# Kernel optimization log

Hardware: AMD Instinct MI355X
Metric: run time of the kernel (lower is better)

The kernel has to match this reference:

```python
import jax, jax.numpy as jnp
import numpy as np

N = 100000
E = 1600000
F_IN = 128
HID = 128
C = 10
NEG_SLOPE = 0.2


def setup_inputs() -> dict:
    key = jax.random.key(0)
    ks = jax.random.split(key, 12)
    x = jax.random.normal(ks[0], (N, F_IN), dtype=jnp.float32)
    edge_index = jax.random.randint(ks[1], (2, E), 0, N, dtype=jnp.int64)
    batch = jnp.zeros((N,), dtype=jnp.int64)
    s1 = 1.0 / np.sqrt(F_IN)
    s2 = 1.0 / np.sqrt(HID)
    return {
        "x": x,
        "edge_index": edge_index,
        "batch": batch,
        "W1": jax.random.normal(ks[2], (F_IN, HID), dtype=jnp.float32) * s1,
        "a_src1": jax.random.normal(ks[3], (HID,), dtype=jnp.float32) * s2,
        "a_dst1": jax.random.normal(ks[4], (HID,), dtype=jnp.float32) * s2,
        "b1": jnp.zeros((HID,), dtype=jnp.float32),
        "W2": jax.random.normal(ks[5], (HID, HID), dtype=jnp.float32) * s2,
        "a_src2": jax.random.normal(ks[6], (HID,), dtype=jnp.float32) * s2,
        "a_dst2": jax.random.normal(ks[7], (HID,), dtype=jnp.float32) * s2,
        "b2": jnp.zeros((HID,), dtype=jnp.float32),
        "Wlin": jax.random.normal(ks[8], (HID, C), dtype=jnp.float32) * s2,
        "blin": jnp.zeros((C,), dtype=jnp.float32),
    }


def gat_conv(x, src, dst, W, a_src, a_dst, b):
    # PyG GATConv, heads=1: h = xW; alpha_e = softmax_dst(leaky_relu(a_src.h[src] + a_dst.h[dst]))
    h = x @ W                                  # [N, H]
    alpha_s = h @ a_src                        # [N]
    alpha_d = h @ a_dst                        # [N]
    e = jax.nn.leaky_relu(alpha_s[src] + alpha_d[dst], NEG_SLOPE)  # [E]
    m = jax.ops.segment_max(e, dst, num_segments=N)                # per-dst max (stable softmax)
    ex = jnp.exp(e - m[dst])
    denom = jax.ops.segment_sum(ex, dst, num_segments=N)
    alpha = ex / (denom[dst] + 1e-16)          # [E]
    out = jax.ops.segment_sum(h[src] * alpha[:, None], dst, num_segments=N)
    return out + b


def reference(x, edge_index, batch, W1, a_src1, a_dst1, b1, W2, a_src2, a_dst2, b2, Wlin, blin):
    x = x.astype(jnp.float32)
    loops = jnp.arange(N, dtype=edge_index.dtype)
    src = jnp.concatenate([edge_index[0], loops])  # add_self_loops=True
    dst = jnp.concatenate([edge_index[1], loops])
    h = jax.nn.relu(gat_conv(x, src, dst, W1, a_src1, a_dst1, b1))
    h = jax.nn.relu(gat_conv(h, src, dst, W2, a_src2, a_dst2, b2))
    # dropout(p=0.5) is identity in eval mode
    return h @ Wlin + blin
```

## Files before the change

kernel.cpp:

```cpp
#include <hip/hip_runtime.h>

#define N_NODES 100000
#define N_EDGES 1600000
#define TOTE    (N_EDGES + N_NODES)
#define NEG     0.2f
#define NB      ((N_NODES + 255) >> 8)

typedef __attribute__((ext_vector_type(8))) short bf16x8;
typedef __attribute__((ext_vector_type(4))) float floatx4;

__device__ __forceinline__ unsigned short f2bf(float f) {
  unsigned int u = __float_as_uint(f);
  u += 0x7fffu + ((u >> 16) & 1u);
  return (unsigned short)(u >> 16);
}
__device__ __forceinline__ float bf_lo(unsigned int r) { return __uint_as_float(r << 16); }
__device__ __forceinline__ float bf_hi(unsigned int r) { return __uint_as_float(r & 0xffff0000u); }

__global__ __launch_bounds__(256) void k_zero_bcnt(int* __restrict__ bucketCnt) {
  for (int i = threadIdx.x; i < NB * 16; i += 256) bucketCnt[i] = 0;
}

__global__ __launch_bounds__(256) void k_bucket_hist(const int* __restrict__ ei, int* __restrict__ bucketCnt) {
  __shared__ int h[NB];
  int t = threadIdx.x;
  for (int b = t; b < NB; b += 256) h[b] = 0;
  __syncthreads();
#pragma unroll
  for (int j = 0; j < 16; ++j) {
    int idx = blockIdx.x * 4096 + j * 256 + t;
    if (idx < N_EDGES) atomicAdd(&h[ei[N_EDGES + idx] >> 8], 1);
  }
  __syncthreads();
  for (int b = t; b < NB; b += 256) { int v = h[b]; if (v) atomicAdd(&bucketCnt[b * 16], v); }
}

__global__ __launch_bounds__(512) void k_bin_scan(const int* __restrict__ bucketCnt,
                                                  int* __restrict__ binOffs, int* __restrict__ binCursor) {
  __shared__ int sc[512];
  int t = threadIdx.x;
  int v = (t < NB) ? bucketCnt[t * 16] : 0;
  sc[t] = v; __syncthreads();
  for (int off = 1; off < 512; off <<= 1) {
    int x = (t >= off) ? sc[t - off] : 0;
    __syncthreads();
    sc[t] += x;
    __syncthreads();
  }
  int excl = sc[t] - v;
  if (t <= NB) binOffs[t] = excl;
  if (t < NB) binCursor[t * 16] = excl;
}

__global__ __launch_bounds__(256) void k_binA(const int* __restrict__ ei, int* __restrict__ binCursor,
                                              unsigned int* __restrict__ binned) {
  __shared__ int hist[NB];
  __shared__ int cur[NB];
  int t = threadIdx.x;
  for (int b = t; b < NB; b += 256) hist[b] = 0;
  __syncthreads();
  unsigned int pk[16]; int bk[16];
#pragma unroll
  for (int j = 0; j < 16; ++j) {
    int idx = blockIdx.x * 4096 + j * 256 + t;
    if (idx < N_EDGES) {
      int s = ei[idx], d = ei[N_EDGES + idx];
      bk[j] = d >> 8;
      pk[j] = ((unsigned int)s << 8) | (unsigned int)(d & 255);
      atomicAdd(&hist[bk[j]], 1);
    } else bk[j] = -1;
  }
  __syncthreads();
  for (int b = t; b < NB; b += 256) {
    int h = hist[b];
    if (h) cur[b] = atomicAdd(&binCursor[b * 16], h);
  }
  __syncthreads();
#pragma unroll
  for (int j = 0; j < 16; ++j) {
    if (bk[j] >= 0) {
      int pos = atomicAdd(&cur[bk[j]], 1);
      binned[pos] = pk[j];
    }
  }
}

__global__ __launch_bounds__(256) void k_binB(const unsigned int* __restrict__ binned,
                                              const int* __restrict__ binOffs,
                                              int* __restrict__ offs, int* __restrict__ srcs) {
  __shared__ int cnt[256];
  __shared__ int sc[256];
  __shared__ int cur[256];
  int b = blockIdx.x;
  int t = threadIdx.x;
  int node0 = b << 8;
  int nNodes = min(256, N_NODES - node0);
  int e0 = binOffs[b], e1 = binOffs[b + 1];
  int base = e0 + node0;

  cnt[t] = 0; __syncthreads();
  for (int i = e0 + t; i < e1; i += 256) atomicAdd(&cnt[binned[i] & 255u], 1);
  __syncthreads();

  int v = (t < nNodes) ? cnt[t] + 1 : 0;
  sc[t] = v; __syncthreads();
  for (int off = 1; off < 256; off <<= 1) {
    int x = (t >= off) ? sc[t - off] : 0;
    __syncthreads();
    sc[t] += x;
    __syncthreads();
  }
  int excl = sc[t] - v;
  if (t < nNodes) {
    offs[node0 + t] = base + excl;
    srcs[base + excl] = node0 + t;
  }
  cur[t] = excl + 1;
  __syncthreads();

  for (int i = e0 + t; i < e1; i += 256) {
    unsigned int e = binned[i];
    int j = (int)(e & 255u);
    int s = (int)(e >> 8);
    int p = atomicAdd(&cur[j], 1);
    srcs[base + p] = s;
  }
  if (b == 0 && t == 0) offs[N_NODES] = TOTE;
}

__global__ __launch_bounds__(256) void k_wprep(const float* __restrict__ W1, const float* __restrict__ W2,
                                               unsigned short* __restrict__ B1hi, unsigned short* __restrict__ B1lo,
                                               unsigned short* __restrict__ B2hi, unsigned short* __restrict__ B2lo) {
  int b = blockIdx.x;
  const float* W = (b < 8) ? W1 : W2;
  unsigned short* Bh = (b < 8) ? B1hi : B2hi;
  unsigned short* Bl = (b < 8) ? B1lo : B2lo;
  int ntile = b & 7;
  int t = threadIdx.x;
  int kq = t >> 6, lane = t & 63;
  int q = lane >> 4, m = lane & 15;
  int n = ntile * 16 + m;
  union { unsigned short us[8]; uint4 u4; } hi, lo;
#pragma unroll
  for (int j = 0; j < 8; ++j) {
    int k = kq * 32 + q * 8 + j;
    float w = W[(size_t)k * 128 + n];
    unsigned int u = __float_as_uint(w);
    hi.us[j] = (unsigned short)(u >> 16);
    float res = w - __uint_as_float(u & 0xffff0000u);
    lo.us[j] = f2bf(res);
  }
  size_t fo = ((size_t)(ntile * 4 + kq) * 64 + lane) * 8;
  *reinterpret_cast<uint4*>(Bh + fo) = hi.u4;
  *reinterpret_cast<uint4*>(Bl + fo) = lo.u4;
}

template <bool SPLIT>
__global__ __launch_bounds__(256) void k_gemm_mfma(const void* __restrict__ Aptr,
                                                   const unsigned short* __restrict__ Bhi,
                                                   const unsigned short* __restrict__ Blo,
                                                   unsigned short* __restrict__ Cb,
                                                   const float* __restrict__ avS, const float* __restrict__ avD,
                                                   float* __restrict__ aS, float* __restrict__ aD,
                                                   float* __restrict__ slotS, float* __restrict__ slotD) {
  __shared__ unsigned short sC[128 * 136];
  __shared__ float redS[128 * 2], redD[128 * 2];
  __shared__ float mS[128], mD[128];
  int t = threadIdx.x;
  int w = t >> 6, lane = t & 63;
  int q = lane >> 4, m = lane & 15;
  int wr = (w >> 1) * 64, wc = (w & 1) * 64;
  int rbase = blockIdx.x * 128;

  floatx4 acc[4][4];
#pragma unroll
  for (int mt = 0; mt < 4; ++mt)
#pragma unroll
    for (int nt = 0; nt < 4; ++nt) acc[mt][nt] = (floatx4){0.f, 0.f, 0.f, 0.f};

#pragma unroll
  for (int k0 = 0; k0 < 4; ++k0) {
    bf16x8 Bh[4], Bl[4], Ah[4], Al[4];
#pragma unroll
    for (int nt = 0; nt < 4; ++nt) {
      int ntg = (w & 1) * 4 + nt;
      size_t fo = ((size_t)(ntg * 4 + k0) * 64 + lane) * 8;
      Bh[nt] = *reinterpret_cast<const bf16x8*>(Bhi + fo);
      Bl[nt] = *reinterpret_cast<const bf16x8*>(Blo + fo);
    }
#pragma unroll
    for (int mt = 0; mt < 4; ++mt) {
      int row = rbase + wr + mt * 16 + m;
      row = min(row, N_NODES - 1);
      if constexpr (SPLIT) {
        const float* ap = (const float*)Aptr + (size_t)row * 128 + k0 * 32 + q * 8;
        float4 v0 = *reinterpret_cast<const float4*>(ap);
        float4 v1 = *reinterpret_cast<const float4*>(ap + 4);
        float av[8] = {v0.x, v0.y, v0.z, v0.w, v1.x, v1.y, v1.z, v1.w};
        union { unsigned short us[8]; bf16x8 v; } uh, ul;
#pragma unroll
        for (int j = 0; j < 8; ++j) {
          unsigned int u = __float_as_uint(av[j]);
          uh.us[j] = (unsigned short)(u >> 16);
          float res = av[j] - __uint_as_float(u & 0xffff0000u);
          ul.us[j] = f2bf(res);
        }
        Ah[mt] = uh.v; Al[mt] = ul.v;
      } else {
        const unsigned short* ap = (const unsigned short*)Aptr + (size_t)row * 128 + k0 * 32 + q * 8;
        Ah[mt] = *reinterpret_cast<const bf16x8*>(ap);
      }
    }
#pragma unroll
    for (int mt = 0; mt < 4; ++mt)
#pragma unroll
      for (int nt = 0; nt < 4; ++nt) {
        acc[mt][nt] = __builtin_amdgcn_mfma_f32_16x16x32_bf16(Ah[mt], Bh[nt], acc[mt][nt], 0, 0, 0);
        acc[mt][nt] = __builtin_amdgcn_mfma_f32_16x16x32_bf16(Ah[mt], Bl[nt], acc[mt][nt], 0, 0, 0);
        if constexpr (SPLIT)
          acc[mt][nt] = __builtin_amdgcn_mfma_f32_16x16x32_bf16(Al[mt], Bh[nt], acc[mt][nt], 0, 0, 0);
      }
  }

  float avs[4], avd[4];
#pragma unroll
  for (int nt = 0; nt < 4; ++nt) {
    int c = wc + nt * 16 + m;
    avs[nt] = avS[c];
    avd[nt] = avD[c];
  }
#pragma unroll
  for (int mt = 0; mt < 4; ++mt)
#pragma unroll
    for (int r = 0; r < 4; ++r) {
      float ps = 0.f, pd = 0.f;
#pragma unroll
      for (int nt = 0; nt < 4; ++nt) {
        float cv = acc[mt][nt][r];
        ps += cv * avs[nt];
        pd += cv * avd[nt];
      }
      ps += __shfl_xor(ps, 1); pd += __shfl_xor(pd, 1);
      ps += __shfl_xor(ps, 2); pd += __shfl_xor(pd, 2);
      ps += __shfl_xor(ps, 4); pd += __shfl_xor(pd, 4);
      ps += __shfl_xor(ps, 8); pd += __shfl_xor(pd, 8);
      if (m == 0) {
        int rl = wr + mt * 16 + q * 4 + r;
        redS[rl * 2 + (w & 1)] = ps;
        redD[rl * 2 + (w & 1)] = pd;
      }
    }

#pragma unroll
  for (int mt = 0; mt < 4; ++mt)
#pragma unroll
    for (int nt = 0; nt < 4; ++nt)
#pragma unroll
      for (int r = 0; r < 4; ++r) {
        int rl = wr + mt * 16 + q * 4 + r;
        int cl = wc + nt * 16 + m;
        sC[rl * 136 + cl] = f2bf(acc[mt][nt][r]);
      }
  __syncthreads();

#pragma unroll
  for (int i = 0; i < 8; ++i) {
    int idx = i * 256 + t;
    int rl = idx >> 4, kk = idx & 15;
    int gr = rbase + rl;
    if (gr < N_NODES)
      *reinterpret_cast<uint4*>(Cb + (size_t)gr * 128 + kk * 8) =
          *reinterpret_cast<const uint4*>(sC + rl * 136 + kk * 8);
  }

  if (t < 128) {
    int gr = rbase + t;
    bool ok = gr < N_NODES;
    float ps = redS[t * 2] + redS[t * 2 + 1];
    float pd = redD[t * 2] + redD[t * 2 + 1];
    if (ok) { aS[gr] = ps; aD[gr] = pd; }
    mS[t] = ok ? ps : -1e30f;
    mD[t] = ok ? pd : -1e30f;
  }
  __syncthreads();
#pragma unroll
  for (int off = 64; off > 0; off >>= 1) {
    if (t < off) { mS[t] = fmaxf(mS[t], mS[t + off]); mD[t] = fmaxf(mD[t], mD[t + off]); }
    __syncthreads();
  }
  if (t == 0) { slotS[blockIdx.x] = mS[0]; slotD[blockIdx.x] = mD[0]; }
}

__global__ __launch_bounds__(256) void k_gmax(const float* __restrict__ slotS,
                                              const float* __restrict__ slotD,
                                              int n, float* __restrict__ gMh) {
  __shared__ float sS[256], sD[256];
  int t = threadIdx.x;
  float ms = -1e30f, md = -1e30f;
  for (int i = t; i < n; i += 256) { ms = fmaxf(ms, slotS[i]); md = fmaxf(md, slotD[i]); }
  sS[t] = ms; sD[t] = md;
  __syncthreads();
#pragma unroll
  for (int off = 128; off > 0; off >>= 1) {
    if (t < off) { sS[t] = fmaxf(sS[t], sS[t + off]); sD[t] = fmaxf(sD[t], sD[t + off]); }
    __syncthreads();
  }
  if (t == 0) {
    float M = sS[0] + sD[0];
    gMh[0] = (M > 0.f) ? M : NEG * M;
  }
}

#define FMA8(E, R)                                     \
  do {                                                 \
    acc[0] += (E) * bf_lo((R).x); acc[1] += (E) * bf_hi((R).x); \
    acc[2] += (E) * bf_lo((R).y); acc[3] += (E) * bf_hi((R).y); \
    acc[4] += (E) * bf_lo((R).z); acc[5] += (E) * bf_hi((R).z); \
    acc[6] += (E) * bf_lo((R).w); acc[7] += (E) * bf_hi((R).w); \
  } while (0)

__global__ __launch_bounds__(256) void k_aggregate(const unsigned short* __restrict__ hb,
                                                   const float* __restrict__ aS,
                                                   const float* __restrict__ aD,
                                                   const int* __restrict__ offs,
                                                   const int* __restrict__ srcs,
                                                   const float* __restrict__ bias,
                                                   const float* __restrict__ gMh,
                                                   unsigned short* __restrict__ outb) {
  __shared__ float2 pairs[16 * 17];
  int t = threadIdx.x;
  int g = t >> 4;
  int l = t & 15;
  int dst = blockIdx.x * 16 + g;
  float Mh = gMh[0];
  int beg = offs[dst], end = offs[dst + 1];
  float adn = aD[dst];
  float denom = 0.f;
  float acc[8];
#pragma unroll
  for (int k = 0; k < 8; ++k) acc[k] = 0.f;
  const int pbase = g * 17;

  for (int chunk = beg; chunk < end; chunk += 16) {
    int i = chunk + l;
    float ex = 0.f; int s = 0;
    if (i < end) {
      s = srcs[i];
      float e = aS[s] + adn;
      e = (e > 0.f) ? e : NEG * e;
      ex = __expf(e - Mh);
    }
    denom += ex;
    pairs[pbase + l] = make_float2(ex, __int_as_float(s));
    int cnt = min(16, end - chunk);
    int j = 0;
    for (; j + 4 <= cnt; j += 4) {
      float2 p0 = pairs[pbase + j + 0];
      float2 p1 = pairs[pbase + j + 1];
      float2 p2 = pairs[pbase + j + 2];
      float2 p3 = pairs[pbase + j + 3];
      uint4 r0 = *reinterpret_cast<const uint4*>(hb + (size_t)__float_as_int(p0.y) * 128 + l * 8);
      uint4 r1 = *reinterpret_cast<const uint4*>(hb + (size_t)__float_as_int(p1.y) * 128 + l * 8);
      uint4 r2 = *reinterpret_cast<const uint4*>(hb + (size_t)__float_as_int(p2.y) * 128 + l * 8);
      uint4 r3 = *reinterpret_cast<const uint4*>(hb + (size_t)__float_as_int(p3.y) * 128 + l * 8);
      FMA8(p0.x, r0);
      FMA8(p1.x, r1);
      FMA8(p2.x, r2);
      FMA8(p3.x, r3);
    }
    for (; j < cnt; ++j) {
      float2 pp = pairs[pbase + j];
      uint4 r = *reinterpret_cast<const uint4*>(hb + (size_t)__float_as_int(pp.y) * 128 + l * 8);
      FMA8(pp.x, r);
    }
  }
  denom += __shfl_xor(denom, 1);
  denom += __shfl_xor(denom, 2);
  denom += __shfl_xor(denom, 4);
  denom += __shfl_xor(denom, 8);
  float inv = 1.f / (denom + 1e-16f);
  float4 b0 = *reinterpret_cast<const float4*>(bias + l * 8);
  float4 b1 = *reinterpret_cast<const float4*>(bias + l * 8 + 4);
  float o0 = fmaxf(acc[0] * inv + b0.x, 0.f), o1 = fmaxf(acc[1] * inv + b0.y, 0.f);
  float o2 = fmaxf(acc[2] * inv + b0.z, 0.f), o3 = fmaxf(acc[3] * inv + b0.w, 0.f);
  float o4 = fmaxf(acc[4] * inv + b1.x, 0.f), o5 = fmaxf(acc[5] * inv + b1.y, 0.f);
  float o6 = fmaxf(acc[6] * inv + b1.z, 0.f), o7 = fmaxf(acc[7] * inv + b1.w, 0.f);
  union { unsigned short us[8]; uint4 u4; } oo;
  oo.us[0] = f2bf(o0); oo.us[1] = f2bf(o1); oo.us[2] = f2bf(o2); oo.us[3] = f2bf(o3);
  oo.us[4] = f2bf(o4); oo.us[5] = f2bf(o5); oo.us[6] = f2bf(o6); oo.us[7] = f2bf(o7);
  *reinterpret_cast<uint4*>(outb + (size_t)dst * 128 + l * 8) = oo.u4;
}

#define UNPK(V, B)                                     \
  do {                                                 \
    h[(B)+0] = bf_lo((V).x); h[(B)+1] = bf_hi((V).x);  \
    h[(B)+2] = bf_lo((V).y); h[(B)+3] = bf_hi((V).y);  \
    h[(B)+4] = bf_lo((V).z); h[(B)+5] = bf_hi((V).z);  \
    h[(B)+6] = bf_lo((V).w); h[(B)+7] = bf_hi((V).w);  \
  } while (0)

__global__ __launch_bounds__(256) void k_linear(const unsigned short* __restrict__ hb,
                                                const float* __restrict__ Wl,
                                                const float* __restrict__ bl,
                                                float* __restrict__ out) {
  __shared__ float sWt[10 * 144];
  __shared__ float sbl[10];
  int t = threadIdx.x;
  if (t < 128) {
    int jj = t >> 5, ii = t & 31;
#pragma unroll
    for (int c = 0; c < 10; ++c) sWt[c * 144 + jj * 36 + ii] = Wl[t * 10 + c];
  }
  if (t < 10) sbl[t] = bl[t];
  __syncthreads();
  int node = blockIdx.x * 64 + (t >> 2);
  int j = t & 3;
  if (node >= N_NODES) return;
  const unsigned short* hrow = hb + (size_t)node * 128 + j * 32;
  uint4 v0 = *reinterpret_cast<const uint4*>(hrow);
  uint4 v1 = *reinterpret_cast<const uint4*>(hrow + 8);
  uint4 v2 = *reinterpret_cast<const uint4*>(hrow + 16);
  uint4 v3 = *reinterpret_cast<const uint4*>(hrow + 24);
  float h[32];
  UNPK(v0, 0); UNPK(v1, 8); UNPK(v2, 16); UNPK(v3, 24);
  float p[10];
#pragma unroll
  for (int c = 0; c < 10; ++c) {
    const float4* wp = reinterpret_cast<const float4*>(&sWt[c * 144 + j * 36]);
    float s = 0.f;
#pragma unroll
    for (int qq = 0; qq < 8; ++qq) {
      float4 wv = wp[qq];
      s += h[qq * 4 + 0] * wv.x + h[qq * 4 + 1] * wv.y + h[qq * 4 + 2] * wv.z + h[qq * 4 + 3] * wv.w;
    }
    p[c] = s;
  }
#pragma unroll
  for (int c = 0; c < 10; ++c) {
    p[c] += __shfl_xor(p[c], 1);
    p[c] += __shfl_xor(p[c], 2);
  }
  if (j == 0) {
    float* orow = out + (size_t)node * 10;
    *reinterpret_cast<float2*>(orow + 0) = make_float2(p[0] + sbl[0], p[1] + sbl[1]);
    *reinterpret_cast<float2*>(orow + 2) = make_float2(p[2] + sbl[2], p[3] + sbl[3]);
    *reinterpret_cast<float2*>(orow + 4) = make_float2(p[4] + sbl[4], p[5] + sbl[5]);
    *reinterpret_cast<float2*>(orow + 6) = make_float2(p[6] + sbl[6], p[7] + sbl[7]);
    *reinterpret_cast<float2*>(orow + 8) = make_float2(p[8] + sbl[8], p[9] + sbl[9]);
  }
}

extern "C" void kernel_launch(void* const* d_in, const int* in_sizes, int n_in,
                              void* d_out, int out_size, void* d_ws, size_t ws_size,
                              hipStream_t stream) {
  const float* x   = (const float*)d_in[0];
  const int*   ei  = (const int*)d_in[1];
  const float* W1  = (const float*)d_in[3];
  const float* as1 = (const float*)d_in[4];
  const float* ad1 = (const float*)d_in[5];
  const float* b1  = (const float*)d_in[6];
  const float* W2  = (const float*)d_in[7];
  const float* as2 = (const float*)d_in[8];
  const float* ad2 = (const float*)d_in[9];
  const float* b2  = (const float*)d_in[10];
  const float* Wl  = (const float*)d_in[11];
  const float* bl  = (const float*)d_in[12];
  float* out = (float*)d_out;

  char* p = (char*)d_ws;
  unsigned short* hb   = (unsigned short*)p; p += (size_t)N_NODES * 128 * sizeof(unsigned short);
  unsigned short* hagg = (unsigned short*)p; p += (size_t)N_NODES * 128 * sizeof(unsigned short);
  float* aS    = (float*)p; p += (size_t)N_NODES * sizeof(float);
  float* aD    = (float*)p; p += (size_t)N_NODES * sizeof(float);
  int* offs    = (int*)p;   p += (size_t)(N_NODES + 4) * sizeof(int);
  int* srcs    = (int*)p;   p += (size_t)TOTE * sizeof(int);
  int* bucketCnt = (int*)p; p += (size_t)NB * 16 * sizeof(int);
  int* binOffs   = (int*)p; p += (size_t)(NB + 4) * sizeof(int);
  int* binCursor = (int*)p; p += (size_t)NB * 16 * sizeof(int);
  float* slotS = (float*)p; p += 1024 * sizeof(float);
  float* slotD = (float*)p; p += 1024 * sizeof(float);
  float* gMh = (float*)p;   p += 4 * sizeof(float);
  unsigned short* B1hi = (unsigned short*)p; p += 128 * 128 * sizeof(unsigned short);
  unsigned short* B1lo = (unsigned short*)p; p += 128 * 128 * sizeof(unsigned short);
  unsigned short* B2hi = (unsigned short*)p; p += 128 * 128 * sizeof(unsigned short);
  unsigned short* B2lo = (unsigned short*)p; p += 128 * 128 * sizeof(unsigned short);
  unsigned int* binned = (unsigned int*)hagg;

  int binBlocks = (N_EDGES + 4095) / 4096;

  k_wprep<<<16, 256, 0, stream>>>(W1, W2, B1hi, B1lo, B2hi, B2lo);
  k_zero_bcnt<<<1, 256, 0, stream>>>(bucketCnt);
  k_bucket_hist<<<binBlocks, 256, 0, stream>>>(ei, bucketCnt);
  k_bin_scan<<<1, 512, 0, stream>>>(bucketCnt, binOffs, binCursor);
  k_binA<<<binBlocks, 256, 0, stream>>>(ei, binCursor, binned);
  k_binB<<<NB, 256, 0, stream>>>(binned, binOffs, offs, srcs);

  int gemmBlocks = (N_NODES + 127) / 128;
  int aggBlocks  = N_NODES / 16;
  int linBlocks  = (N_NODES + 63) / 64;

  k_gemm_mfma<true><<<gemmBlocks, 256, 0, stream>>>(x, B1hi, B1lo, hb, as1, ad1, aS, aD, slotS, slotD);
  k_gmax<<<1, 256, 0, stream>>>(slotS, slotD, gemmBlocks, gMh);
  k_aggregate<<<aggBlocks, 256, 0, stream>>>(hb, aS, aD, offs, srcs, b1, gMh, hagg);
  k_gemm_mfma<false><<<gemmBlocks, 256, 0, stream>>>(hagg, B2hi, B2lo, hb, as2, ad2, aS, aD, slotS, slotD);
  k_gmax<<<1, 256, 0, stream>>>(slotS, slotD, gemmBlocks, gMh);
  k_aggregate<<<aggBlocks, 256, 0, stream>>>(hb, aS, aD, offs, srcs, b2, gMh, hagg);
  k_linear<<<linBlocks, 256, 0, stream>>>(hagg, Wl, bl, out);
}
```

Measured before the change: 375.7 us.

## Degree-sort destination nodes, fuse final linear into aggregate, widen gather unroll

Builds a degree histogram in binB and a counting-sort permutation of destination nodes so that each aggregate block processes nodes of similar degree, reducing divergence between the 16-lane groups in a block. The second aggregate now applies the 128x10 classifier directly from registers via a pre-transposed Wl and shuffle reductions, removing the k_linear kernel and the bf16 round-trip of the final hidden layer. The gather loop gains an 8-way unrolled path for more loads in flight. This adds two small preprocessing kernels and scattered output writes from the permutation order.

```diff
diff --git a/kernel.cpp b/kernel.cpp
--- a/kernel.cpp
+++ b/kernel.cpp
@@ -17,8 +17,9 @@
 __device__ __forceinline__ float bf_lo(unsigned int r) { return __uint_as_float(r << 16); }
 __device__ __forceinline__ float bf_hi(unsigned int r) { return __uint_as_float(r & 0xffff0000u); }
 
-__global__ __launch_bounds__(256) void k_zero_bcnt(int* __restrict__ bucketCnt) {
+__global__ __launch_bounds__(256) void k_zero_bcnt(int* __restrict__ bucketCnt, int* __restrict__ degHist) {
   for (int i = threadIdx.x; i < NB * 16; i += 256) bucketCnt[i] = 0;
+  for (int i = threadIdx.x; i < 64 * 16; i += 256) degHist[i] = 0;
 }
 
 __global__ __launch_bounds__(256) void k_bucket_hist(const int* __restrict__ ei, int* __restrict__ bucketCnt) {
@@ -87,10 +88,12 @@
 
 __global__ __launch_bounds__(256) void k_binB(const unsigned int* __restrict__ binned,
                                               const int* __restrict__ binOffs,
-                                              int* __restrict__ offs, int* __restrict__ srcs) {
+                                              int* __restrict__ offs, int* __restrict__ srcs,
+                                              int* __restrict__ degHist) {
   __shared__ int cnt[256];
   __shared__ int sc[256];
   __shared__ int cur[256];
+  __shared__ int dh[64];
   int b = blockIdx.x;
   int t = threadIdx.x;
   int node0 = b << 8;
@@ -98,7 +101,9 @@
   int e0 = binOffs[b], e1 = binOffs[b + 1];
   int base = e0 + node0;
 
-  cnt[t] = 0; __syncthreads();
+  cnt[t] = 0;
+  if (t < 64) dh[t] = 0;
+  __syncthreads();
   for (int i = e0 + t; i < e1; i += 256) atomicAdd(&cnt[binned[i] & 255u], 1);
   __syncthreads();
 
@@ -114,9 +119,11 @@
   if (t < nNodes) {
     offs[node0 + t] = base + excl;
     srcs[base + excl] = node0 + t;
+    atomicAdd(&dh[min(v, 63)], 1);
   }
   cur[t] = excl + 1;
   __syncthreads();
+  if (t < 64) { int x = dh[t]; if (x) atomicAdd(&degHist[t * 16], x); }
 
   for (int i = e0 + t; i < e1; i += 256) {
     unsigned int e = binned[i];
@@ -128,15 +135,58 @@
   if (b == 0 && t == 0) offs[N_NODES] = TOTE;
 }
 
+__global__ void k_pscan(const int* __restrict__ degHist, int* __restrict__ permCur) {
+  if (threadIdx.x == 0 && blockIdx.x == 0) {
+    int run = 0;
+    for (int i = 0; i < 64; ++i) { int v = degHist[i * 16]; permCur[i * 16] = run; run += v; }
+  }
+}
+
+__global__ __launch_bounds__(256) void k_pscat(const int* __restrict__ offs, int* __restrict__ permCur,
+                                               int* __restrict__ permDst, int* __restrict__ begP,
+                                               int* __restrict__ endP) {
+  __shared__ int hist[64];
+  __shared__ int cur[64];
+  int t = threadIdx.x;
+  if (t < 64) hist[t] = 0;
+  __syncthreads();
+  int node = blockIdx.x * 256 + t;
+  int beg = 0, end = 0, bin = -1;
+  if (node < N_NODES) {
+    beg = offs[node];
+    end = offs[node + 1];
+    bin = min(end - beg, 63);
+    atomicAdd(&hist[bin], 1);
+  }
+  __syncthreads();
+  if (t < 64) { int h = hist[t]; if (h) cur[t] = atomicAdd(&permCur[t * 16], h); }
+  __syncthreads();
+  if (bin >= 0) {
+    int pos = atomicAdd(&cur[bin], 1);
+    permDst[pos] = node;
+    begP[pos] = beg;
+    endP[pos] = end;
+  }
+}
+
 __global__ __launch_bounds__(256) void k_wprep(const float* __restrict__ W1, const float* __restrict__ W2,
+                                               const float* __restrict__ Wl,
                                                unsigned short* __restrict__ B1hi, unsigned short* __restrict__ B1lo,
-                                               unsigned short* __restrict__ B2hi, unsigned short* __restrict__ B2lo) {
+                                               unsigned short* __restrict__ B2hi, unsigned short* __restrict__ B2lo,
+                                               float* __restrict__ WlT) {
   int b = blockIdx.x;
+  int t = threadIdx.x;
+  if (b == 16) {
+    for (int i = t; i < 1280; i += 256) {
+      int c = i >> 7, k = i & 127;
+      WlT[i] = Wl[k * 10 + c];
+    }
+    return;
+  }
   const float* W = (b < 8) ? W1 : W2;
   unsigned short* Bh = (b < 8) ? B1hi : B2hi;
   unsigned short* Bl = (b < 8) ? B1lo : B2lo;
   int ntile = b & 7;
-  int t = threadIdx.x;
   int kq = t >> 6, lane = t & 63;
   int q = lane >> 4, m = lane & 15;
   int n = ntile * 16 + m;
@@ -319,21 +369,28 @@
     acc[6] += (E) * bf_lo((R).w); acc[7] += (E) * bf_hi((R).w); \
   } while (0)
 
+template <bool FUSECLS>
 __global__ __launch_bounds__(256) void k_aggregate(const unsigned short* __restrict__ hb,
                                                    const float* __restrict__ aS,
                                                    const float* __restrict__ aD,
-                                                   const int* __restrict__ offs,
+                                                   const int* __restrict__ permDst,
+                                                   const int* __restrict__ begP,
+                                                   const int* __restrict__ endP,
                                                    const int* __restrict__ srcs,
                                                    const float* __restrict__ bias,
                                                    const float* __restrict__ gMh,
-                                                   unsigned short* __restrict__ outb) {
+                                                   unsigned short* __restrict__ outb,
+                                                   const float* __restrict__ WlT,
+                                                   const float* __restrict__ bl,
+                                                   float* __restrict__ out) {
   __shared__ float2 pairs[16 * 17];
   int t = threadIdx.x;
   int g = t >> 4;
   int l = t & 15;
-  int dst = blockIdx.x * 16 + g;
+  int idx = blockIdx.x * 16 + g;
   float Mh = gMh[0];
-  int beg = offs[dst], end = offs[dst + 1];
+  int dst = permDst[idx];
+  int beg = begP[idx], end = endP[idx];
   float adn = aD[dst];
   float denom = 0.f;
   float acc[8];
@@ -354,19 +411,25 @@
     pairs[pbase + l] = make_float2(ex, __int_as_float(s));
     int cnt = min(16, end - chunk);
     int j = 0;
+    for (; j + 8 <= cnt; j += 8) {
+      float2 pp[8]; uint4 rr[8];
+#pragma unroll
+      for (int u = 0; u < 8; ++u) pp[u] = pairs[pbase + j + u];
+#pragma unroll
+      for (int u = 0; u < 8; ++u)
+        rr[u] = *reinterpret_cast<const uint4*>(hb + (size_t)__float_as_int(pp[u].y) * 128 + l * 8);
+#pragma unroll
+      for (int u = 0; u < 8; ++u) FMA8(pp[u].x, rr[u]);
+    }
     for (; j + 4 <= cnt; j += 4) {
-      float2 p0 = pairs[pbase + j + 0];
-      float2 p1 = pairs[pbase + j + 1];
-      float2 p2 = pairs[pbase + j + 2];
-      float2 p3 = pairs[pbase + j + 3];
-      uint4 r0 = *reinterpret_cast<const uint4*>(hb + (size_t)__float_as_int(p0.y) * 128 + l * 8);
-      uint4 r1 = *reinterpret_cast<const uint4*>(hb + (size_t)__float_as_int(p1.y) * 128 + l * 8);
-      uint4 r2 = *reinterpret_cast<const uint4*>(hb + (size_t)__float_as_int(p2.y) * 128 + l * 8);
-      uint4 r3 = *reinterpret_cast<const uint4*>(hb + (size_t)__float_as_int(p3.y) * 128 + l * 8);
-      FMA8(p0.x, r0);
-      FMA8(p1.x, r1);
-      FMA8(p2.x, r2);
-      FMA8(p3.x, r3);
+      float2 pp[4]; uint4 rr[4];
+#pragma unroll
+      for (int u = 0; u < 4; ++u) pp[u] = pairs[pbase + j + u];
+#pragma unroll
+      for (int u = 0; u < 4; ++u)
+        rr[u] = *reinterpret_cast<const uint4*>(hb + (size_t)__float_as_int(pp[u].y) * 128 + l * 8);
+#pragma unroll
+      for (int u = 0; u < 4; ++u) FMA8(pp[u].x, rr[u]);
     }
     for (; j < cnt; ++j) {
       float2 pp = pairs[pbase + j];
@@ -385,68 +448,41 @@
   float o2 = fmaxf(acc[2] * inv + b0.z, 0.f), o3 = fmaxf(acc[3] * inv + b0.w, 0.f);
   float o4 = fmaxf(acc[4] * inv + b1.x, 0.f), o5 = fmaxf(acc[5] * inv + b1.y, 0.f);
   float o6 = fmaxf(acc[6] * inv + b1.z, 0.f), o7 = fmaxf(acc[7] * inv + b1.w, 0.f);
-  union { unsigned short us[8]; uint4 u4; } oo;
-  oo.us[0] = f2bf(o0); oo.us[1] = f2bf(o1); oo.us[2] = f2bf(o2); oo.us[3] = f2bf(o3);
-  oo.us[4] = f2bf(o4); oo.us[5] = f2bf(o5); oo.us[6] = f2bf(o6); oo.us[7] = f2bf(o7);
-  *reinterpret_cast<uint4*>(outb + (size_t)dst * 128 + l * 8) = oo.u4;
-}
-
-#define UNPK(V, B)                                     \
-  do {                                                 \
-    h[(B)+0] = bf_lo((V).x); h[(B)+1] = bf_hi((V).x);  \
-    h[(B)+2] = bf_lo((V).y); h[(B)+3] = bf_hi((V).y);  \
-    h[(B)+4] = bf_lo((V).z); h[(B)+5] = bf_hi((V).z);  \
-    h[(B)+6] = bf_lo((V).w); h[(B)+7] = bf_hi((V).w);  \
-  } while (0)
-
-__global__ __launch_bounds__(256) void k_linear(const unsigned short* __restrict__ hb,
-                                                const float* __restrict__ Wl,
-                                                const float* __restrict__ bl,
-                                                float* __restrict__ out) {
-  __shared__ float sWt[10 * 144];
-  __shared__ float sbl[10];
-  int t = threadIdx.x;
-  if (t < 128) {
-    int jj = t >> 5, ii = t & 31;
-#pragma unroll
-    for (int c = 0; c < 10; ++c) sWt[c * 144 + jj * 36 + ii] = Wl[t * 10 + c];
-  }
-  if (t < 10) sbl[t] = bl[t];
-  __syncthreads();
-  int node = blockIdx.x * 64 + (t >> 2);
-  int j = t & 3;
-  if (node >= N_NODES) return;
-  const unsigned short* hrow = hb + (size_t)node * 128 + j * 32;
-  uint4 v0 = *reinterpret_cast<const uint4*>(hrow);
-  uint4 v1 = *reinterpret_cast<const uint4*>(hrow + 8);
-  uint4 v2 = *reinterpret_cast<const uint4*>(hrow + 16);
-  uint4 v3 = *reinterpret_cast<const uint4*>(hrow + 24);
-  float h[32];
-  UNPK(v0, 0); UNPK(v1, 8); UNPK(v2, 16); UNPK(v3, 24);
-  float p[10];
-#pragma unroll
-  for (int c = 0; c < 10; ++c) {
-    const float4* wp = reinterpret_cast<const float4*>(&sWt[c * 144 + j * 36]);
-    float s = 0.f;
-#pragma unroll
-    for (int qq = 0; qq < 8; ++qq) {
-      float4 wv = wp[qq];
-      s += h[qq * 4 + 0] * wv.x + h[qq * 4 + 1] * wv.y + h[qq * 4 + 2] * wv.z + h[qq * 4 + 3] * wv.w;
-    }
-    p[c] = s;
-  }
-#pragma unroll
-  for (int c = 0; c < 10; ++c) {
-    p[c] += __shfl_xor(p[c], 1);
-    p[c] += __shfl_xor(p[c], 2);
-  }
-  if (j == 0) {
-    float* orow = out + (size_t)node * 10;
-    *reinterpret_cast<float2*>(orow + 0) = make_float2(p[0] + sbl[0], p[1] + sbl[1]);
-    *reinterpret_cast<float2*>(orow + 2) = make_float2(p[2] + sbl[2], p[3] + sbl[3]);
-    *reinterpret_cast<float2*>(orow + 4) = make_float2(p[4] + sbl[4], p[5] + sbl[5]);
-    *reinterpret_cast<float2*>(orow + 6) = make_float2(p[6] + sbl[6], p[7] + sbl[7]);
-    *reinterpret_cast<float2*>(orow + 8) = make_float2(p[8] + sbl[8], p[9] + sbl[9]);
+
+  if constexpr (!FUSECLS) {
+    union { unsigned short us[8]; uint4 u4; } oo;
+    oo.us[0] = f2bf(o0); oo.us[1] = f2bf(o1); oo.us[2] = f2bf(o2); oo.us[3] = f2bf(o3);
+    oo.us[4] = f2bf(o4); oo.us[5] = f2bf(o5); oo.us[6] = f2bf(o6); oo.us[7] = f2bf(o7);
+    *reinterpret_cast<uint4*>(outb + (size_t)dst * 128 + l * 8) = oo.u4;
+  } else {
+    float p[10];
+#pragma unroll
+    for (int c = 0; c < 10; ++c) {
+      const float4* wp = reinterpret_cast<const float4*>(WlT + c * 128 + l * 8);
+      float4 w0 = wp[0], w1 = wp[1];
+      p[c] = o0 * w0.x + o1 * w0.y + o2 * w0.z + o3 * w0.w
+           + o4 * w1.x + o5 * w1.y + o6 * w1.z + o7 * w1.w;
+    }
+#pragma unroll
+    for (int c = 0; c < 10; ++c) {
+      p[c] += __shfl_xor(p[c], 1);
+      p[c] += __shfl_xor(p[c], 2);
+      p[c] += __shfl_xor(p[c], 4);
+      p[c] += __shfl_xor(p[c], 8);
+    }
+    if (l == 0) {
+      float* orow = out + (size_t)dst * 10;
+      float2 bb0 = *reinterpret_cast<const float2*>(bl + 0);
+      float2 bb1 = *reinterpret_cast<const float2*>(bl + 2);
+      float2 bb2 = *reinterpret_cast<const float2*>(bl + 4);
+      float2 bb3 = *reinterpret_cast<const float2*>(bl + 6);
+      float2 bb4 = *reinterpret_cast<const float2*>(bl + 8);
+      *reinterpret_cast<float2*>(orow + 0) = make_float2(p[0] + bb0.x, p[1] + bb0.y);
+      *reinterpret_cast<float2*>(orow + 2) = make_float2(p[2] + bb1.x, p[3] + bb1.y);
+      *reinterpret_cast<float2*>(orow + 4) = make_float2(p[4] + bb2.x, p[5] + bb2.y);
+      *reinterpret_cast<float2*>(orow + 6) = make_float2(p[6] + bb3.x, p[7] + bb3.y);
+      *reinterpret_cast<float2*>(orow + 8) = make_float2(p[8] + bb4.x, p[9] + bb4.y);
+    }
   }
 }
 
@@ -477,6 +513,11 @@
   int* bucketCnt = (int*)p; p += (size_t)NB * 16 * sizeof(int);
   int* binOffs   = (int*)p; p += (size_t)(NB + 4) * sizeof(int);
   int* binCursor = (int*)p; p += (size_t)NB * 16 * sizeof(int);
+  int* degHist   = (int*)p; p += 64 * 16 * sizeof(int);
+  int* permCur   = (int*)p; p += 64 * 16 * sizeof(int);
+  int* permDst   = (int*)p; p += (size_t)N_NODES * sizeof(int);
+  int* begP      = (int*)p; p += (size_t)N_NODES * sizeof(int);
+  int* endP      = (int*)p; p += (size_t)N_NODES * sizeof(int);
   float* slotS = (float*)p; p += 1024 * sizeof(float);
   float* slotD = (float*)p; p += 1024 * sizeof(float);
   float* gMh = (float*)p;   p += 4 * sizeof(float);
@@ -484,26 +525,30 @@
   unsigned short* B1lo = (unsigned short*)p; p += 128 * 128 * sizeof(unsigned short);
   unsigned short* B2hi = (unsigned short*)p; p += 128 * 128 * sizeof(unsigned short);
   unsigned short* B2lo = (unsigned short*)p; p += 128 * 128 * sizeof(unsigned short);
+  float* WlT = (float*)p;   p += 1280 * sizeof(float);
   unsigned int* binned = (unsigned int*)hagg;
 
   int binBlocks = (N_EDGES + 4095) / 4096;
-
-  k_wprep<<<16, 256, 0, stream>>>(W1, W2, B1hi, B1lo, B2hi, B2lo);
-  k_zero_bcnt<<<1, 256, 0, stream>>>(bucketCnt);
+  int nodeBlocks = (N_NODES + 255) / 256;
+
+  k_wprep<<<17, 256, 0, stream>>>(W1, W2, Wl, B1hi, B1lo, B2hi, B2lo, WlT);
+  k_zero_bcnt<<<1, 256, 0, stream>>>(bucketCnt, degHist);
   k_bucket_hist<<<binBlocks, 256, 0, stream>>>(ei, bucketCnt);
   k_bin_scan<<<1, 512, 0, stream>>>(bucketCnt, binOffs, binCursor);
   k_binA<<<binBlocks, 256, 0, stream>>>(ei, binCursor, binned);
-  k_binB<<<NB, 256, 0, stream>>>(binned, binOffs, offs, srcs);
+  k_binB<<<NB, 256, 0, stream>>>(binned, binOffs, offs, srcs, degHist);
+  k_pscan<<<1, 64, 0, stream>>>(degHist, permCur);
+  k_pscat<<<nodeBlocks, 256, 0, stream>>>(offs, permCur, permDst, begP, endP);
 
   int gemmBlocks = (N_NODES + 127) / 128;
   int aggBlocks  = N_NODES / 16;
-  int linBlocks  = (N_NODES + 63) / 64;
 
   k_gemm_mfma<true><<<gemmBlocks, 256, 0, stream>>>(x, B1hi, B1lo, hb, as1, ad1, aS, aD, slotS, slotD);
   k_gmax<<<1, 256, 0, stream>>>(slotS, slotD, gemmBlocks, gMh);
-  k_aggregate<<<aggBlocks, 256, 0, stream>>>(hb, aS, aD, offs, srcs, b1, gMh, hagg);
+  k_aggregate<false><<<aggBlocks, 256, 0, stream>>>(hb, aS, aD, permDst, begP, endP, srcs, b1, gMh,
+                                                    hagg, nullptr, nullptr, nullptr);
   k_gemm_mfma<false><<<gemmBlocks, 256, 0, stream>>>(hagg, B2hi, B2lo, hb, as2, ad2, aS, aD, slotS, slotD);
   k_gmax<<<1, 256, 0, stream>>>(slotS, slotD, gemmBlocks, gMh);
-  k_aggregate<<<aggBlocks, 256, 0, stream>>>(hb, aS, aD, offs, srcs, b2, gMh, hagg);
-  k_linear<<<linBlocks, 256, 0, stream>>>(hagg, Wl, bl, out);
-}
+  k_aggregate<true><<<aggBlocks, 256, 0, stream>>>(hb, aS, aD, permDst, begP, endP, srcs, b2, gMh,
+                                                   nullptr, WlT, bl, out);
+}
```

Measured after the change: 390.6 us. +4.0%, slower.

## Fuse final linear classifier into second aggregation and shrink GEMM row tile

Applied to the files above, without the earlier changes.

The final 128->10 linear layer now runs inside the second aggregation kernel. Each 16-lane group dots its relu'd outputs against a transposed Wl prepared in the weight-prep kernel, which removes the k_linear launch and the bf16 hidden-state write and re-read. The GEMM kernel also drops its row tile from 128 to 64 rows per block, with each wave covering 32 columns, so it launches twice as many blocks with less LDS and fewer accumulators each. That should improve occupancy, at the cost of more block-max slots and loading the A tile once per wave.

```diff
diff --git a/kernel.cpp b/kernel.cpp
--- a/kernel.cpp
+++ b/kernel.cpp
@@ -129,14 +129,23 @@
 }
 
 __global__ __launch_bounds__(256) void k_wprep(const float* __restrict__ W1, const float* __restrict__ W2,
+                                               const float* __restrict__ Wl,
                                                unsigned short* __restrict__ B1hi, unsigned short* __restrict__ B1lo,
-                                               unsigned short* __restrict__ B2hi, unsigned short* __restrict__ B2lo) {
+                                               unsigned short* __restrict__ B2hi, unsigned short* __restrict__ B2lo,
+                                               float* __restrict__ WlT) {
   int b = blockIdx.x;
+  int t = threadIdx.x;
+  if (b == 16) {
+    for (int i = t; i < 1280; i += 256) {
+      int c = i >> 7, k = i & 127;
+      WlT[i] = Wl[k * 10 + c];
+    }
+    return;
+  }
   const float* W = (b < 8) ? W1 : W2;
   unsigned short* Bh = (b < 8) ? B1hi : B2hi;
   unsigned short* Bl = (b < 8) ? B1lo : B2lo;
   int ntile = b & 7;
-  int t = threadIdx.x;
   int kq = t >> 6, lane = t & 63;
   int q = lane >> 4, m = lane & 15;
   int n = ntile * 16 + m;
@@ -163,34 +172,33 @@
                                                    const float* __restrict__ avS, const float* __restrict__ avD,
                                                    float* __restrict__ aS, float* __restrict__ aD,
                                                    float* __restrict__ slotS, float* __restrict__ slotD) {
-  __shared__ unsigned short sC[128 * 136];
-  __shared__ float redS[128 * 2], redD[128 * 2];
-  __shared__ float mS[128], mD[128];
+  __shared__ unsigned short sC[64 * 136];
+  __shared__ float redS[64 * 4], redD[64 * 4];
+  __shared__ float mS[64], mD[64];
   int t = threadIdx.x;
   int w = t >> 6, lane = t & 63;
   int q = lane >> 4, m = lane & 15;
-  int wr = (w >> 1) * 64, wc = (w & 1) * 64;
-  int rbase = blockIdx.x * 128;
-
-  floatx4 acc[4][4];
+  int rbase = blockIdx.x * 64;
+
+  floatx4 acc[4][2];
 #pragma unroll
   for (int mt = 0; mt < 4; ++mt)
 #pragma unroll
-    for (int nt = 0; nt < 4; ++nt) acc[mt][nt] = (floatx4){0.f, 0.f, 0.f, 0.f};
+    for (int nt = 0; nt < 2; ++nt) acc[mt][nt] = (floatx4){0.f, 0.f, 0.f, 0.f};
 
 #pragma unroll
   for (int k0 = 0; k0 < 4; ++k0) {
-    bf16x8 Bh[4], Bl[4], Ah[4], Al[4];
-#pragma unroll
-    for (int nt = 0; nt < 4; ++nt) {
-      int ntg = (w & 1) * 4 + nt;
+    bf16x8 Bh[2], Bl[2], Ah[4], Al[4];
+#pragma unroll
+    for (int nt = 0; nt < 2; ++nt) {
+      int ntg = w * 2 + nt;
       size_t fo = ((size_t)(ntg * 4 + k0) * 64 + lane) * 8;
       Bh[nt] = *reinterpret_cast<const bf16x8*>(Bhi + fo);
       Bl[nt] = *reinterpret_cast<const bf16x8*>(Blo + fo);
     }
 #pragma unroll
     for (int mt = 0; mt < 4; ++mt) {
-      int row = rbase + wr + mt * 16 + m;
+      int row = rbase + mt * 16 + m;
       row = min(row, N_NODES - 1);
       if constexpr (SPLIT) {
         const float* ap = (const float*)Aptr + (size_t)row * 128 + k0 * 32 + q * 8;
@@ -214,7 +222,7 @@
 #pragma unroll
     for (int mt = 0; mt < 4; ++mt)
 #pragma unroll
-      for (int nt = 0; nt < 4; ++nt) {
+      for (int nt = 0; nt < 2; ++nt) {
         acc[mt][nt] = __builtin_amdgcn_mfma_f32_16x16x32_bf16(Ah[mt], Bh[nt], acc[mt][nt], 0, 0, 0);
         acc[mt][nt] = __builtin_amdgcn_mfma_f32_16x16x32_bf16(Ah[mt], Bl[nt], acc[mt][nt], 0, 0, 0);
         if constexpr (SPLIT)
@@ -222,10 +230,10 @@
       }
   }
 
-  float avs[4], avd[4];
-#pragma unroll
-  for (int nt = 0; nt < 4; ++nt) {
-    int c = wc + nt * 16 + m;
+  float avs[2], avd[2];
+#pragma unroll
+  for (int nt = 0; nt < 2; ++nt) {
+    int c = w * 32 + nt * 16 + m;
     avs[nt] = avS[c];
     avd[nt] = avD[c];
   }
@@ -233,38 +241,33 @@
   for (int mt = 0; mt < 4; ++mt)
 #pragma unroll
     for (int r = 0; r < 4; ++r) {
-      float ps = 0.f, pd = 0.f;
-#pragma unroll
-      for (int nt = 0; nt < 4; ++nt) {
-        float cv = acc[mt][nt][r];
-        ps += cv * avs[nt];
-        pd += cv * avd[nt];
-      }
+      float ps = acc[mt][0][r] * avs[0] + acc[mt][1][r] * avs[1];
+      float pd = acc[mt][0][r] * avd[0] + acc[mt][1][r] * avd[1];
       ps += __shfl_xor(ps, 1); pd += __shfl_xor(pd, 1);
       ps += __shfl_xor(ps, 2); pd += __shfl_xor(pd, 2);
       ps += __shfl_xor(ps, 4); pd += __shfl_xor(pd, 4);
       ps += __shfl_xor(ps, 8); pd += __shfl_xor(pd, 8);
       if (m == 0) {
-        int rl = wr + mt * 16 + q * 4 + r;
-        redS[rl * 2 + (w & 1)] = ps;
-        redD[rl * 2 + (w & 1)] = pd;
+        int rl = mt * 16 + q * 4 + r;
+        redS[rl * 4 + w] = ps;
+        redD[rl * 4 + w] = pd;
       }
     }
 
 #pragma unroll
   for (int mt = 0; mt < 4; ++mt)
 #pragma unroll
-    for (int nt = 0; nt < 4; ++nt)
+    for (int nt = 0; nt < 2; ++nt)
 #pragma unroll
       for (int r = 0; r < 4; ++r) {
-        int rl = wr + mt * 16 + q * 4 + r;
-        int cl = wc + nt * 16 + m;
+        int rl = mt * 16 + q * 4 + r;
+        int cl = w * 32 + nt * 16 + m;
         sC[rl * 136 + cl] = f2bf(acc[mt][nt][r]);
       }
   __syncthreads();
 
 #pragma unroll
-  for (int i = 0; i < 8; ++i) {
+  for (int i = 0; i < 4; ++i) {
     int idx = i * 256 + t;
     int rl = idx >> 4, kk = idx & 15;
     int gr = rbase + rl;
@@ -273,18 +276,18 @@
           *reinterpret_cast<const uint4*>(sC + rl * 136 + kk * 8);
   }
 
-  if (t < 128) {
+  if (t < 64) {
     int gr = rbase + t;
     bool ok = gr < N_NODES;
-    float ps = redS[t * 2] + redS[t * 2 + 1];
-    float pd = redD[t * 2] + redD[t * 2 + 1];
+    float ps = redS[t * 4] + redS[t * 4 + 1] + redS[t * 4 + 2] + redS[t * 4 + 3];
+    float pd = redD[t * 4] + redD[t * 4 + 1] + redD[t * 4 + 2] + redD[t * 4 + 3];
     if (ok) { aS[gr] = ps; aD[gr] = pd; }
     mS[t] = ok ? ps : -1e30f;
     mD[t] = ok ? pd : -1e30f;
   }
   __syncthreads();
 #pragma unroll
-  for (int off = 64; off > 0; off >>= 1) {
+  for (int off = 32; off > 0; off >>= 1) {
     if (t < off) { mS[t] = fmaxf(mS[t], mS[t + off]); mD[t] = fmaxf(mD[t], mD[t + off]); }
     __syncthreads();
   }
@@ -319,6 +322,7 @@
     acc[6] += (E) * bf_lo((R).w); acc[7] += (E) * bf_hi((R).w); \
   } while (0)
 
+template <bool FUSECLS>
 __global__ __launch_bounds__(256) void k_aggregate(const unsigned short* __restrict__ hb,
                                                    const float* __restrict__ aS,
                                                    const float* __restrict__ aD,
@@ -326,7 +330,10 @@
                                                    const int* __restrict__ srcs,
                                                    const float* __restrict__ bias,
                                                    const float* __restrict__ gMh,
-                                                   unsigned short* __restrict__ outb) {
+                                                   unsigned short* __restrict__ outb,
+                                                   const float* __restrict__ WlT,
+                                                   const float* __restrict__ bl,
+                                                   float* __restrict__ out) {
   __shared__ float2 pairs[16 * 17];
   int t = threadIdx.x;
   int g = t >> 4;
@@ -385,68 +392,41 @@
   float o2 = fmaxf(acc[2] * inv + b0.z, 0.f), o3 = fmaxf(acc[3] * inv + b0.w, 0.f);
   float o4 = fmaxf(acc[4] * inv + b1.x, 0.f), o5 = fmaxf(acc[5] * inv + b1.y, 0.f);
   float o6 = fmaxf(acc[6] * inv + b1.z, 0.f), o7 = fmaxf(acc[7] * inv + b1.w, 0.f);
-  union { unsigned short us[8]; uint4 u4; } oo;
-  oo.us[0] = f2bf(o0); oo.us[1] = f2bf(o1); oo.us[2] = f2bf(o2); oo.us[3] = f2bf(o3);
-  oo.us[4] = f2bf(o4); oo.us[5] = f2bf(o5); oo.us[6] = f2bf(o6); oo.us[7] = f2bf(o7);
-  *reinterpret_cast<uint4*>(outb + (size_t)dst * 128 + l * 8) = oo.u4;
-}
-
-#define UNPK(V, B)                                     \
-  do {                                                 \
-    h[(B)+0] = bf_lo((V).x); h[(B)+1] = bf_hi((V).x);  \
-    h[(B)+2] = bf_lo((V).y); h[(B)+3] = bf_hi((V).y);  \
-    h[(B)+4] = bf_lo((V).z); h[(B)+5] = bf_hi((V).z);  \
-    h[(B)+6] = bf_lo((V).w); h[(B)+7] = bf_hi((V).w);  \
-  } while (0)
-
-__global__ __launch_bounds__(256) void k_linear(const unsigned short* __restrict__ hb,
-                                                const float* __restrict__ Wl,
-                                                const float* __restrict__ bl,
-                                                float* __restrict__ out) {
-  __shared__ float sWt[10 * 144];
-  __shared__ float sbl[10];
-  int t = threadIdx.x;
-  if (t < 128) {
-    int jj = t >> 5, ii = t & 31;
-#pragma unroll
-    for (int c = 0; c < 10; ++c) sWt[c * 144 + jj * 36 + ii] = Wl[t * 10 + c];
-  }
-  if (t < 10) sbl[t] = bl[t];
-  __syncthreads();
-  int node = blockIdx.x * 64 + (t >> 2);
-  int j = t & 3;
-  if (node >= N_NODES) return;
-  const unsigned short* hrow = hb + (size_t)node * 128 + j * 32;
-  uint4 v0 = *reinterpret_cast<const uint4*>(hrow);
-  uint4 v1 = *reinterpret_cast<const uint4*>(hrow + 8);
-  uint4 v2 = *reinterpret_cast<const uint4*>(hrow + 16);
-  uint4 v3 = *reinterpret_cast<const uint4*>(hrow + 24);
-  float h[32];
-  UNPK(v0, 0); UNPK(v1, 8); UNPK(v2, 16); UNPK(v3, 24);
-  float p[10];
-#pragma unroll
-  for (int c = 0; c < 10; ++c) {
-    const float4* wp = reinterpret_cast<const float4*>(&sWt[c * 144 + j * 36]);
-    float s = 0.f;
-#pragma unroll
-    for (int qq = 0; qq < 8; ++qq) {
-      float4 wv = wp[qq];
-      s += h[qq * 4 + 0] * wv.x + h[qq * 4 + 1] * wv.y + h[qq * 4 + 2] * wv.z + h[qq * 4 + 3] * wv.w;
-    }
-    p[c] = s;
-  }
-#pragma unroll
-  for (int c = 0; c < 10; ++c) {
-    p[c] += __shfl_xor(p[c], 1);
-    p[c] += __shfl_xor(p[c], 2);
-  }
-  if (j == 0) {
-    float* orow = out + (size_t)node * 10;
-    *reinterpret_cast<float2*>(orow + 0) = make_float2(p[0] + sbl[0], p[1] + sbl[1]);
-    *reinterpret_cast<float2*>(orow + 2) = make_float2(p[2] + sbl[2], p[3] + sbl[3]);
-    *reinterpret_cast<float2*>(orow + 4) = make_float2(p[4] + sbl[4], p[5] + sbl[5]);
-    *reinterpret_cast<float2*>(orow + 6) = make_float2(p[6] + sbl[6], p[7] + sbl[7]);
-    *reinterpret_cast<float2*>(orow + 8) = make_float2(p[8] + sbl[8], p[9] + sbl[9]);
+
+  if constexpr (!FUSECLS) {
+    union { unsigned short us[8]; uint4 u4; } oo;
+    oo.us[0] = f2bf(o0); oo.us[1] = f2bf(o1); oo.us[2] = f2bf(o2); oo.us[3] = f2bf(o3);
+    oo.us[4] = f2bf(o4); oo.us[5] = f2bf(o5); oo.us[6] = f2bf(o6); oo.us[7] = f2bf(o7);
+    *reinterpret_cast<uint4*>(outb + (size_t)dst * 128 + l * 8) = oo.u4;
+  } else {
+    float p[10];
+#pragma unroll
+    for (int c = 0; c < 10; ++c) {
+      const float4* wp = reinterpret_cast<const float4*>(WlT + c * 128 + l * 8);
+      float4 w0 = wp[0], w1 = wp[1];
+      p[c] = o0 * w0.x + o1 * w0.y + o2 * w0.z + o3 * w0.w
+           + o4 * w1.x + o5 * w1.y + o6 * w1.z + o7 * w1.w;
+    }
+#pragma unroll
+    for (int c = 0; c < 10; ++c) {
+      p[c] += __shfl_xor(p[c], 1);
+      p[c] += __shfl_xor(p[c], 2);
+      p[c] += __shfl_xor(p[c], 4);
+      p[c] += __shfl_xor(p[c], 8);
+    }
+    if (l == 0) {
+      float* orow = out + (size_t)dst * 10;
+      float2 bb0 = *reinterpret_cast<const float2*>(bl + 0);
+      float2 bb1 = *reinterpret_cast<const float2*>(bl + 2);
+      float2 bb2 = *reinterpret_cast<const float2*>(bl + 4);
+      float2 bb3 = *reinterpret_cast<const float2*>(bl + 6);
+      float2 bb4 = *reinterpret_cast<const float2*>(bl + 8);
+      *reinterpret_cast<float2*>(orow + 0) = make_float2(p[0] + bb0.x, p[1] + bb0.y);
+      *reinterpret_cast<float2*>(orow + 2) = make_float2(p[2] + bb1.x, p[3] + bb1.y);
+      *reinterpret_cast<float2*>(orow + 4) = make_float2(p[4] + bb2.x, p[5] + bb2.y);
+      *reinterpret_cast<float2*>(orow + 6) = make_float2(p[6] + bb3.x, p[7] + bb3.y);
+      *reinterpret_cast<float2*>(orow + 8) = make_float2(p[8] + bb4.x, p[9] + bb4.y);
+    }
   }
 }
 
@@ -477,33 +457,34 @@
   int* bucketCnt = (int*)p; p += (size_t)NB * 16 * sizeof(int);
   int* binOffs   = (int*)p; p += (size_t)(NB + 4) * sizeof(int);
   int* binCursor = (int*)p; p += (size_t)NB * 16 * sizeof(int);
-  float* slotS = (float*)p; p += 1024 * sizeof(float);
-  float* slotD = (float*)p; p += 1024 * sizeof(float);
+  float* slotS = (float*)p; p += 2048 * sizeof(float);
+  float* slotD = (float*)p; p += 2048 * sizeof(float);
   float* gMh = (float*)p;   p += 4 * sizeof(float);
   unsigned short* B1hi = (unsigned short*)p; p += 128 * 128 * sizeof(unsigned short);
   unsigned short* B1lo = (unsigned short*)p; p += 128 * 128 * sizeof(unsigned short);
   unsigned short* B2hi = (unsigned short*)p; p += 128 * 128 * sizeof(unsigned short);
   unsigned short* B2lo = (unsigned short*)p; p += 128 * 128 * sizeof(unsigned short);
+  float* WlT = (float*)p;   p += 1280 * sizeof(float);
   unsigned int* binned = (unsigned int*)hagg;
 
   int binBlocks = (N_EDGES + 4095) / 4096;
 
-  k_wprep<<<16, 256, 0, stream>>>(W1, W2, B1hi, B1lo, B2hi, B2lo);
+  k_wprep<<<17, 256, 0, stream>>>(W1, W2, Wl, B1hi, B1lo, B2hi, B2lo, WlT);
   k_zero_bcnt<<<1, 256, 0, stream>>>(bucketCnt);
   k_bucket_hist<<<binBlocks, 256, 0, stream>>>(ei, bucketCnt);
   k_bin_scan<<<1, 512, 0, stream>>>(bucketCnt, binOffs, binCursor);
   k_binA<<<binBlocks, 256, 0, stream>>>(ei, binCursor, binned);
   k_binB<<<NB, 256, 0, stream>>>(binned, binOffs, offs, srcs);
 
-  int gemmBlocks = (N_NODES + 127) / 128;
+  int gemmBlocks = (N_NODES + 63) / 64;
   int aggBlocks  = N_NODES / 16;
-  int linBlocks  = (N_NODES + 63) / 64;
 
   k_gemm_mfma<true><<<gemmBlocks, 256, 0, stream>>>(x, B1hi, B1lo, hb, as1, ad1, aS, aD, slotS, slotD);
   k_gmax<<<1, 256, 0, stream>>>(slotS, slotD, gemmBlocks, gMh);
-  k_aggregate<<<aggBlocks, 256, 0, stream>>>(hb, aS, aD, offs, srcs, b1, gMh, hagg);
+  k_aggregate<false><<<aggBlocks, 256, 0, stream>>>(hb, aS, aD, offs, srcs, b1, gMh,
+                                                    hagg, nullptr, nullptr, nullptr);
   k_gemm_mfma<false><<<gemmBlocks, 256, 0, stream>>>(hagg, B2hi, B2lo, hb, as2, ad2, aS, aD, slotS, slotD);
   k_gmax<<<1, 256, 0, stream>>>(slotS, slotD, gemmBlocks, gMh);
-  k_aggregate<<<aggBlocks, 256, 0, stream>>>(hb, aS, aD, offs, srcs, b2, gMh, hagg);
-  k_linear<<<linBlocks, 256, 0, stream>>>(hagg, Wl, bl, out);
-}
+  k_aggregate<true><<<aggBlocks, 256, 0, stream>>>(hb, aS, aD, offs, srcs, b2, gMh,
+                                                   nullptr, WlT, bl, out);
+}
```

Result: slower. 389.9 us (+3.8%).
